# Kernel optimization log

Measured on AMD Instinct MI355X. Metric: run time of the kernel, lower is better.

The kernel has to match this reference:

```python
import jax, jax.numpy as jnp
import numpy as np

NUM_EXPERTS = 8
TOP_K = 2

def setup_inputs() -> dict:
    key = jax.random.key(0)
    ks = jax.random.split(key, 7)
    T, D, H, E = 4096, 1024, 4096, NUM_EXPERTS
    s_in = (2.0 / (D + H)) ** 0.5   # xavier-ish scale for W1
    s_out = (2.0 / (H + D)) ** 0.5
    return {
        "x": jax.random.normal(ks[0], (T, D), jnp.float32),
        "Wg": jax.random.normal(ks[1], (D, E), jnp.float32) * 0.02,
        "bg": jnp.zeros((E,), jnp.float32),
        "W1": jax.random.normal(ks[2], (E, D, H), jnp.float32) * s_in,
        "b1": jnp.zeros((E, H), jnp.float32),
        "W2": jax.random.normal(ks[3], (E, H, D), jnp.float32) * s_out,
        "b2": jnp.zeros((E, D), jnp.float32),
    }

def reference(x, Wg, bg, W1, b1, W2, b2):
    # x: [T, D]; gate over E experts
    gate = jax.nn.softmax(x @ Wg + bg, axis=-1)            # [T, E]
    _, top_idx = jax.lax.top_k(gate, TOP_K)                # [T, K]
    # mask[t, e] = True iff expert e is among top-k for token t
    mask = jnp.any(top_idx[:, :, None] == jnp.arange(NUM_EXPERTS)[None, None, :], axis=1)
    combine_w = jnp.where(mask, gate, 0.0)                 # [T, E]
    # out = sum_e combine_w[:, e] * MLP_e(x); non-selected tokens get weight 0
    out = jnp.zeros_like(x)
    for e in range(NUM_EXPERTS):  # small fixed expert loop
        h = jax.nn.relu(x @ W1[e] + b1[e])                 # [T, H]
        y = h @ W2[e] + b2[e]                              # [T, D]
        out = out + combine_w[:, e:e + 1] * y
    return out
```

## Files before the change

kernel.cpp:

```cpp
#include <hip/hip_runtime.h>
#include <stdint.h>

#define T_TOK 4096
#define DDIM  1024
#define HDIM  4096
#define NEXP  8
#define MAXTILES 72

typedef short s16x8  __attribute__((ext_vector_type(8)));
typedef short s16x4  __attribute__((ext_vector_type(4)));
typedef float f32x4t __attribute__((ext_vector_type(4)));

#define GLOAD16(gp, lp) __builtin_amdgcn_global_load_lds( \
    (const __attribute__((address_space(1))) unsigned int*)(gp), \
    (__attribute__((address_space(3))) unsigned int*)(lp), 16, 0, 0)
#define SB0 __builtin_amdgcn_sched_barrier(0)

__device__ __forceinline__ unsigned short f2b(float f){
  unsigned int u = __float_as_uint(f);
  u += 0x7fffu + ((u >> 16) & 1u);
  return (unsigned short)(u >> 16);
}

__device__ __forceinline__ s16x8 lds_frag(const unsigned short* base, int row, int colElem){
  int byte = row*64 + (((colElem*2)) ^ (((row >> 1) & 3) << 4));
  return *(const s16x8*)((const char*)base + byte);
}

__global__ void gate_kernel(const float* __restrict__ x, const float* __restrict__ Wg,
                            const float* __restrict__ bg,
                            int* __restrict__ topk_e, float* __restrict__ topk_w){
  const int t = blockIdx.x;
  const int lane = threadIdx.x;
  const float* xr = x + (size_t)t * DDIM;
  float acc[NEXP];
  #pragma unroll
  for (int e = 0; e < NEXP; ++e) acc[e] = 0.f;
  #pragma unroll 4
  for (int it = 0; it < DDIM/64; ++it){
    int i = it*64 + lane;
    float xi = xr[i];
    const float4* wr = (const float4*)(Wg + (size_t)i * NEXP);
    float4 w0 = wr[0], w1 = wr[1];
    acc[0] += xi*w0.x; acc[1] += xi*w0.y; acc[2] += xi*w0.z; acc[3] += xi*w0.w;
    acc[4] += xi*w1.x; acc[5] += xi*w1.y; acc[6] += xi*w1.z; acc[7] += xi*w1.w;
  }
  #pragma unroll
  for (int e = 0; e < NEXP; ++e){
    float v = acc[e];
    #pragma unroll
    for (int off = 32; off > 0; off >>= 1) v += __shfl_xor(v, off, 64);
    acc[e] = v;
  }
  if (lane == 0){
    float l[NEXP], m = -1e30f;
    #pragma unroll
    for (int e = 0; e < NEXP; ++e){ l[e] = acc[e] + bg[e]; m = fmaxf(m, l[e]); }
    float p[NEXP], s = 0.f;
    #pragma unroll
    for (int e = 0; e < NEXP; ++e){ p[e] = expf(l[e] - m); s += p[e]; }
    float inv = 1.f / s;
    int a1 = 0; float v1 = -1.f;
    #pragma unroll
    for (int e = 0; e < NEXP; ++e){ p[e] *= inv; if (p[e] > v1){ v1 = p[e]; a1 = e; } }
    int a2 = -1; float v2 = -1.f;
    #pragma unroll
    for (int e = 0; e < NEXP; ++e){ if (e == a1) continue; if (p[e] > v2){ v2 = p[e]; a2 = e; } }
    topk_e[2*t]   = a1; topk_w[2*t]   = v1;
    topk_e[2*t+1] = a2; topk_w[2*t+1] = v2;
  }
}

__global__ void route_count(const int* __restrict__ topk_e, const float* __restrict__ topk_w,
                            int* __restrict__ expertList, float* __restrict__ pairW,
                            int* __restrict__ counts){
  const int e = blockIdx.x;
  const int tid = threadIdx.x;
  __shared__ int pfx[256];
  __shared__ int base_s;
  if (tid == 0) base_s = 0;
  __syncthreads();
  for (int c = 0; c < T_TOK/256; ++c){
    int t = c*256 + tid;
    int e0 = topk_e[2*t], e1 = topk_e[2*t+1];
    int sel = 0; float w = 0.f;
    if (e0 == e){ sel = 1; w = topk_w[2*t]; }
    else if (e1 == e){ sel = 1; w = topk_w[2*t+1]; }
    pfx[tid] = sel;
    __syncthreads();
    for (int off = 1; off < 256; off <<= 1){
      int v = (tid >= off) ? pfx[tid - off] : 0;
      __syncthreads();
      pfx[tid] += v;
      __syncthreads();
    }
    if (sel){
      int pos = base_s + pfx[tid] - 1;
      expertList[e*T_TOK + pos] = t;
      pairW[e*T_TOK + pos] = w;
    }
    __syncthreads();
    if (tid == 0) base_s += pfx[255];
    __syncthreads();
  }
  if (tid == 0) counts[e] = base_s;
}

__global__ void plan_kernel(const int* __restrict__ counts, int* __restrict__ nTiles,
                            int* __restrict__ tileExpert, int* __restrict__ tileStart){
  if (blockIdx.x != 0 || threadIdx.x != 0) return;
  int nt = 0;
  for (int e = 0; e < NEXP; ++e){
    int c = counts[e];
    int tcount = (c + 127) >> 7;
    for (int i = 0; i < tcount; ++i){ tileExpert[nt] = e; tileStart[nt] = i*128; ++nt; }
  }
  *nTiles = nt;
}

__global__ void conv_x(const float* __restrict__ x, unsigned short* __restrict__ xb){
  int i = (blockIdx.x*256 + threadIdx.x)*4;
  float4 v = *(const float4*)(x + i);
  s16x4 o;
  o[0] = (short)f2b(v.x); o[1] = (short)f2b(v.y);
  o[2] = (short)f2b(v.z); o[3] = (short)f2b(v.w);
  *(s16x4*)(xb + i) = o;
}

__global__ __launch_bounds__(256)
void transpose_w(const float* __restrict__ W, unsigned short* __restrict__ Wt,
                 int K, int N){
  const int e = blockIdx.z;
  const float* Wb = W + (size_t)e*K*N;
  unsigned short* Wtb = Wt + (size_t)e*K*N;
  const int n0 = blockIdx.x*64, k0 = blockIdx.y*64;
  __shared__ unsigned short t[64][72];
  const int r  = threadIdx.x >> 4;
  const int c4 = (threadIdx.x & 15) * 4;
  #pragma unroll
  for (int i = 0; i < 4; ++i){
    int k = r + i*16;
    float4 v = *(const float4*)(Wb + (size_t)(k0+k)*N + n0 + c4);
    t[c4+0][k] = f2b(v.x); t[c4+1][k] = f2b(v.y);
    t[c4+2][k] = f2b(v.z); t[c4+3][k] = f2b(v.w);
  }
  __syncthreads();
  const int kk = (threadIdx.x & 7) * 8;
  #pragma unroll
  for (int i = 0; i < 2; ++i){
    int n = (threadIdx.x >> 3) + i*32;
    s16x8 v;
    #pragma unroll
    for (int j = 0; j < 8; ++j) v[j] = (short)t[n][kk+j];
    *(s16x8*)(Wtb + (size_t)(n0+n)*K + k0 + kk) = v;
  }
}

template<int LAYER, int KS>
__global__ __launch_bounds__(256, 4)
void moe_gemm(const unsigned short* __restrict__ Abf,
              const unsigned short* __restrict__ Wt,
              const float* __restrict__ bias,
              const int* __restrict__ nTilesPtr,
              const int* __restrict__ tileExpert,
              const int* __restrict__ tileStart,
              const int* __restrict__ counts,
              const int* __restrict__ expertList,
              const float* __restrict__ pairW,
              unsigned short* __restrict__ Hout,
              float* __restrict__ out)
{
  constexpr int KD = (LAYER == 1) ? DDIM : HDIM;
  constexpr int ND = (LAYER == 1) ? HDIM : DDIM;
  constexpr int NB = ND / 128;
  constexpr int NTfull = KD / 32;

  const int nwg = gridDim.x;
  const int b   = blockIdx.x;
  const int q8 = nwg >> 3, r8 = nwg & 7;
  const int xcd = b & 7, ii = b >> 3;
  const int lin = (xcd < r8 ? xcd*(q8+1) : r8*(q8+1) + (xcd-r8)*q8) + ii;
  const int tile = lin / NB;
  const int n0   = (lin % NB) * 128;
  const int kz   = blockIdx.y;

  if (tile >= *nTilesPtr) return;
  const int e   = tileExpert[tile];
  const int ts  = tileStart[tile];
  const int cnt = counts[e];
  const int tid  = threadIdx.x;
  const int lane = tid & 63;
  const int wave = tid >> 6;
  const int wm = (wave >> 1) * 64;
  const int wn = (wave & 1) * 64;

  __shared__ __align__(16) unsigned short As[2][128][32];
  __shared__ __align__(16) unsigned short Bs[2][128][32];
  __shared__ int   tokenBuf[128];
  __shared__ float wBuf[128];

  if (tid < 128){
    int pos = ts + tid;
    int tok = 0; float w = 0.f;
    if (pos < cnt){ tok = expertList[e*T_TOK + pos]; w = pairW[e*T_TOK + pos]; }
    tokenBuf[tid] = tok; wBuf[tid] = w;
  }
  __syncthreads();

  const int srow = tid >> 2;
  const int slot = (tid & 3) ^ ((tid >> 3) & 3);
  const int koff = slot * 8;
  const unsigned short* gA[2];
  const unsigned short* gB[2];
  #pragma unroll
  for (int g = 0; g < 2; ++g){
    const int row = g*64 + srow;
    if (LAYER == 1) gA[g] = Abf + (size_t)tokenBuf[row]*DDIM + koff;
    else            gA[g] = Abf + (size_t)(tile*128 + row)*HDIM + koff;
    gB[g] = Wt + ((size_t)e*ND + n0 + row)*KD + koff;
  }

  auto STAGE = [&](int buf, int ko){
    unsigned short* la = &As[buf][wave*16][0];
    unsigned short* lb = &Bs[buf][wave*16][0];
    #pragma unroll
    for (int g = 0; g < 2; ++g){
      GLOAD16(gA[g] + ko, la + g*2048);
      GLOAD16(gB[g] + ko, lb + g*2048);
    }
  };

  f32x4t acc[4][4] = {};
  const int fr = lane & 15;
  const int fq = lane >> 4;

  const int kt0 = (kz * NTfull) / KS;
  const int kt1 = ((kz + 1) * NTfull) / KS;
  const int NTl = kt1 - kt0;

  STAGE(0, kt0*32);
  SB0; asm volatile("s_waitcnt vmcnt(0)" ::: "memory");
  __builtin_amdgcn_s_barrier();
  SB0;

  int cur = 0;
  for (int t = 0; t < NTl; ++t){
    if (t + 1 < NTl) STAGE(cur ^ 1, (kt0 + t + 1)*32);

    const unsigned short* Ab = &As[cur][0][0];
    const unsigned short* Bb = &Bs[cur][0][0];
    s16x8 bfr[4], afr[4];
    #pragma unroll
    for (int nf = 0; nf < 4; ++nf) bfr[nf] = lds_frag(Bb, wn + nf*16 + fr, fq*8);
    #pragma unroll
    for (int mf = 0; mf < 4; ++mf) afr[mf] = lds_frag(Ab, wm + mf*16 + fr, fq*8);
    __builtin_amdgcn_s_setprio(1);
    #pragma unroll
    for (int mf = 0; mf < 4; ++mf)
      #pragma unroll
      for (int nf = 0; nf < 4; ++nf)
        acc[mf][nf] = __builtin_amdgcn_mfma_f32_16x16x32_bf16(afr[mf], bfr[nf], acc[mf][nf], 0, 0, 0);
    __builtin_amdgcn_s_setprio(0);

    if (t + 1 < NTl){
      SB0; asm volatile("s_waitcnt vmcnt(0)" ::: "memory");
      __builtin_amdgcn_s_barrier();
      SB0;
    }
    cur ^= 1;
  }

  const int rbase = wm + fq*4;
  const int cbase = wn + fr;
  if (LAYER == 1){
    #pragma unroll
    for (int mf = 0; mf < 4; ++mf){
      #pragma unroll
      for (int nf = 0; nf < 4; ++nf){
        int c = cbase + nf*16;
        float bsv = bias[e*HDIM + n0 + c];
        #pragma unroll
        for (int j = 0; j < 4; ++j){
          int rr = rbase + mf*16 + j;
          float v = fmaxf(acc[mf][nf][j] + bsv, 0.f);
          __builtin_nontemporal_store((unsigned short)f2b(v),
              &Hout[(size_t)(tile*128 + rr)*HDIM + n0 + c]);
        }
      }
    }
  } else {
    #pragma unroll
    for (int mf = 0; mf < 4; ++mf){
      #pragma unroll
      for (int j = 0; j < 4; ++j){
        int rr = rbase + mf*16 + j;
        if (ts + rr < cnt){
          int tok = tokenBuf[rr];
          float w = wBuf[rr];
          #pragma unroll
          for (int nf = 0; nf < 4; ++nf){
            int c = cbase + nf*16;
            float v = acc[mf][nf][j];
            if (kz == 0) v += bias[e*DDIM + n0 + c];
            atomicAdd(out + (size_t)tok*DDIM + n0 + c, w * v);
          }
        }
      }
    }
  }
}

extern "C" void kernel_launch(void* const* d_in, const int* in_sizes, int n_in,
                              void* d_out, int out_size, void* d_ws, size_t ws_size,
                              hipStream_t stream){
  const float* x  = (const float*)d_in[0];
  const float* Wg = (const float*)d_in[1];
  const float* bg = (const float*)d_in[2];
  const float* W1 = (const float*)d_in[3];
  const float* b1 = (const float*)d_in[4];
  const float* W2 = (const float*)d_in[5];
  const float* b2 = (const float*)d_in[6];
  float* out = (float*)d_out;

  char* p = (char*)d_ws;
  int*   topk_e     = (int*)p;   p += (size_t)T_TOK*2*sizeof(int);
  float* topk_w     = (float*)p; p += (size_t)T_TOK*2*sizeof(float);
  int*   counts     = (int*)p;   p += 8*sizeof(int);
  int*   nTiles     = (int*)p;   p += 8*sizeof(int);
  int*   tileExpert = (int*)p;   p += 128*sizeof(int);
  int*   tileStart  = (int*)p;   p += 128*sizeof(int);
  int*   expertList = (int*)p;   p += (size_t)NEXP*T_TOK*sizeof(int);
  float* pairW      = (float*)p; p += (size_t)NEXP*T_TOK*sizeof(float);
  p = (char*)(((uintptr_t)p + 255) & ~(uintptr_t)255);
  unsigned short* xb = (unsigned short*)p;
  p += (size_t)T_TOK*DDIM*sizeof(unsigned short);
  p = (char*)(((uintptr_t)p + 255) & ~(uintptr_t)255);
  unsigned short* Wtbuf = (unsigned short*)p;
  p += (size_t)NEXP*DDIM*HDIM*sizeof(unsigned short);
  p = (char*)(((uintptr_t)p + 255) & ~(uintptr_t)255);
  unsigned short* Hact = (unsigned short*)p;

  hipMemsetAsync(d_out, 0, (size_t)T_TOK*DDIM*sizeof(float), stream);
  gate_kernel<<<T_TOK, 64, 0, stream>>>(x, Wg, bg, topk_e, topk_w);
  route_count<<<NEXP, 256, 0, stream>>>(topk_e, topk_w, expertList, pairW, counts);
  plan_kernel<<<1, 1, 0, stream>>>(counts, nTiles, tileExpert, tileStart);
  conv_x<<<T_TOK*DDIM/1024, 256, 0, stream>>>(x, xb);

  transpose_w<<<dim3(HDIM/64, DDIM/64, NEXP), 256, 0, stream>>>(W1, Wtbuf, DDIM, HDIM);
  moe_gemm<1,1><<<dim3(MAXTILES*(HDIM/128), 1), 256, 0, stream>>>(
      xb, Wtbuf, b1, nTiles, tileExpert, tileStart, counts, expertList, pairW, Hact, nullptr);

  transpose_w<<<dim3(DDIM/64, HDIM/64, NEXP), 256, 0, stream>>>(W2, Wtbuf, HDIM, DDIM);
  moe_gemm<2,2><<<dim3(MAXTILES*(DDIM/128), 2), 256, 0, stream>>>(
      Hact, Wtbuf, b2, nTiles, tileExpert, tileStart, counts, expertList, pairW, nullptr, out);
}
```

Measured before the change: 388.8 us.

## Use single-buffered BK=64 tiles instead of double-buffered BK=32 in MoE GEMM

The GEMM main loop moves from a double-buffered K=32 tile to a single LDS buffer with K=64 per iteration, with an 8-slot XOR swizzle for 128-byte rows. Global loads are now issued and waited on before compute in the same iteration, with a second barrier after the MFMAs, so load/compute overlap within a block is gone. In exchange there are half as many iterations and barriers, and LDS use per block is unchanged. The design relies on other resident waves (4 blocks per CU) to hide the latency that prefetching used to cover.

```diff
diff --git a/kernel.cpp b/kernel.cpp
--- a/kernel.cpp
+++ b/kernel.cpp
@@ -23,7 +23,7 @@
 }
 
 __device__ __forceinline__ s16x8 lds_frag(const unsigned short* base, int row, int colElem){
-  int byte = row*64 + (((colElem*2)) ^ (((row >> 1) & 3) << 4));
+  int byte = row*128 + ((colElem*2) ^ ((row & 7) << 4));
   return *(const s16x8*)((const char*)base + byte);
 }
 
@@ -173,7 +173,7 @@
   constexpr int KD = (LAYER == 1) ? DDIM : HDIM;
   constexpr int ND = (LAYER == 1) ? HDIM : DDIM;
   constexpr int NB = ND / 128;
-  constexpr int NTfull = KD / 32;
+  constexpr int NTfull = KD / 64;
 
   const int nwg = gridDim.x;
   const int b   = blockIdx.x;
@@ -194,8 +194,8 @@
   const int wm = (wave >> 1) * 64;
   const int wn = (wave & 1) * 64;
 
-  __shared__ __align__(16) unsigned short As[2][128][32];
-  __shared__ __align__(16) unsigned short Bs[2][128][32];
+  __shared__ __align__(16) unsigned short As[128][64];
+  __shared__ __align__(16) unsigned short Bs[128][64];
   __shared__ int   tokenBuf[128];
   __shared__ float wBuf[128];
 
@@ -207,24 +207,24 @@
   }
   __syncthreads();
 
-  const int srow = tid >> 2;
-  const int slot = (tid & 3) ^ ((tid >> 3) & 3);
+  const int srow = tid >> 3;
+  const int slot = (tid & 7) ^ ((tid >> 3) & 7);
   const int koff = slot * 8;
-  const unsigned short* gA[2];
-  const unsigned short* gB[2];
-  #pragma unroll
-  for (int g = 0; g < 2; ++g){
-    const int row = g*64 + srow;
+  const unsigned short* gA[4];
+  const unsigned short* gB[4];
+  #pragma unroll
+  for (int g = 0; g < 4; ++g){
+    const int row = g*32 + srow;
     if (LAYER == 1) gA[g] = Abf + (size_t)tokenBuf[row]*DDIM + koff;
     else            gA[g] = Abf + (size_t)(tile*128 + row)*HDIM + koff;
     gB[g] = Wt + ((size_t)e*ND + n0 + row)*KD + koff;
   }
 
-  auto STAGE = [&](int buf, int ko){
-    unsigned short* la = &As[buf][wave*16][0];
-    unsigned short* lb = &Bs[buf][wave*16][0];
-    #pragma unroll
-    for (int g = 0; g < 2; ++g){
+  auto STAGE = [&](int ko){
+    unsigned short* la = &As[0][0] + wave*512;
+    unsigned short* lb = &Bs[0][0] + wave*512;
+    #pragma unroll
+    for (int g = 0; g < 4; ++g){
       GLOAD16(gA[g] + ko, la + g*2048);
       GLOAD16(gB[g] + ko, lb + g*2048);
     }
@@ -236,38 +236,40 @@
 
   const int kt0 = (kz * NTfull) / KS;
   const int kt1 = ((kz + 1) * NTfull) / KS;
-  const int NTl = kt1 - kt0;
-
-  STAGE(0, kt0*32);
-  SB0; asm volatile("s_waitcnt vmcnt(0)" ::: "memory");
-  __builtin_amdgcn_s_barrier();
-  SB0;
-
-  int cur = 0;
-  for (int t = 0; t < NTl; ++t){
-    if (t + 1 < NTl) STAGE(cur ^ 1, (kt0 + t + 1)*32);
-
-    const unsigned short* Ab = &As[cur][0][0];
-    const unsigned short* Bb = &Bs[cur][0][0];
-    s16x8 bfr[4], afr[4];
-    #pragma unroll
-    for (int nf = 0; nf < 4; ++nf) bfr[nf] = lds_frag(Bb, wn + nf*16 + fr, fq*8);
-    #pragma unroll
-    for (int mf = 0; mf < 4; ++mf) afr[mf] = lds_frag(Ab, wm + mf*16 + fr, fq*8);
+
+  for (int t = kt0; t < kt1; ++t){
+    STAGE(t*64);
+    SB0; asm volatile("s_waitcnt vmcnt(0)" ::: "memory");
+    __builtin_amdgcn_s_barrier();
+    SB0;
+
+    const unsigned short* Ab = &As[0][0];
+    const unsigned short* Bb = &Bs[0][0];
+    s16x8 afr[4][2], bfr[4][2];
+    #pragma unroll
+    for (int nf = 0; nf < 4; ++nf)
+      #pragma unroll
+      for (int ks = 0; ks < 2; ++ks)
+        bfr[nf][ks] = lds_frag(Bb, wn + nf*16 + fr, ks*32 + fq*8);
+    #pragma unroll
+    for (int mf = 0; mf < 4; ++mf)
+      #pragma unroll
+      for (int ks = 0; ks < 2; ++ks)
+        afr[mf][ks] = lds_frag(Ab, wm + mf*16 + fr, ks*32 + fq*8);
+
     __builtin_amdgcn_s_setprio(1);
     #pragma unroll
-    for (int mf = 0; mf < 4; ++mf)
-      #pragma unroll
-      for (int nf = 0; nf < 4; ++nf)
-        acc[mf][nf] = __builtin_amdgcn_mfma_f32_16x16x32_bf16(afr[mf], bfr[nf], acc[mf][nf], 0, 0, 0);
+    for (int ks = 0; ks < 2; ++ks)
+      #pragma unroll
+      for (int mf = 0; mf < 4; ++mf)
+        #pragma unroll
+        for (int nf = 0; nf < 4; ++nf)
+          acc[mf][nf] = __builtin_amdgcn_mfma_f32_16x16x32_bf16(
+              afr[mf][ks], bfr[nf][ks], acc[mf][nf], 0, 0, 0);
     __builtin_amdgcn_s_setprio(0);
-
-    if (t + 1 < NTl){
-      SB0; asm volatile("s_waitcnt vmcnt(0)" ::: "memory");
-      __builtin_amdgcn_s_barrier();
-      SB0;
-    }
-    cur ^= 1;
+    SB0;
+    __builtin_amdgcn_s_barrier();
+    SB0;
   }
 
   const int rbase = wm + fq*4;
```

After: 710.7 us. 82.8% more time.
